# Optimization experiments

Measured on AMD Instinct MI355X. Metric: run time of the kernel, lower is better.

The kernel has to match this reference:

```python
import jax, jax.numpy as jnp
import numpy as np

B, D, DM, K, KA = 4096, 64, 256, 32, 16


def setup_inputs() -> dict:
    key = jax.random.key(0)
    ks = jax.random.split(key, 20)
    rn = lambda i, shape, s=1.0: jax.random.normal(ks[i], shape, dtype=jnp.float32) * s
    return dict(
        z=rn(0, (B, D)),
        rw=jax.random.uniform(ks[1], (B, K), dtype=jnp.float32),
        action_z=rn(2, (B, D)),
        action_rw=jax.random.uniform(ks[3], (B, KA), dtype=jnp.float32),
        action_code_z=rn(4, (B, D)),
        control=rn(5, (B, D)),
        exact_covector=rn(6, (B, D)),
        chart_emb=rn(7, (K, DM), 0.05),
        chart_anchor=rn(8, (K, D)),
        action_chart_emb=rn(9, (KA, DM), 0.05),
        action_chart_anchor=rn(10, (KA, D)),
        z_embed_W=rn(11, (D, DM), 0.05), z_embed_b=jnp.zeros((DM,), jnp.float32),
        lat_W=rn(12, (D, DM), 0.05), lat_b=jnp.zeros((DM,), jnp.float32),
        code_W=rn(13, (D, DM), 0.05), code_b=jnp.zeros((DM,), jnp.float32),
        Wq=rn(14, (DM, DM), 0.05), Wk=rn(15, (DM, DM), 0.05),
        Wv=rn(16, (DM, DM), 0.05), Wo=rn(17, (DM, DM), 0.05),
        form_W=rn(18, (DM, D), 0.05), form_b=jnp.zeros((D,), jnp.float32),
    )


def _spectral_linear(x, W, b):
    # SpectralLinear: weight normalized by its largest singular value.
    sigma = jnp.linalg.svd(W, compute_uv=False)[0]
    return x @ (W / jnp.maximum(sigma, jnp.float32(1e-8))) + b


def _forward(z, rw, action_z, action_rw, action_code_z, control, exact_covector,
             chart_emb, chart_anchor, action_chart_emb, action_chart_anchor,
             z_embed_W, z_embed_b, lat_W, lat_b, code_W, code_b,
             Wq, Wk, Wv, Wo, form_W, form_b):
    b = z.shape[0]
    # ChartTokenizer: routing-weighted chart embeddings + anchor latents.
    chart_x = rw[:, :, None] * chart_emb[None]                      # [B,K,DM]
    chart_z = jnp.broadcast_to(chart_anchor[None], (b, K, D))       # [B,K,D]
    a_chart_x = action_rw[:, :, None] * action_chart_emb[None]      # [B,KA,DM]
    a_chart_z = jnp.broadcast_to(action_chart_anchor[None], (b, KA, D))
    # LatentTokenizers: single token per latent.
    lat_x = (action_z @ lat_W + lat_b)[:, None, :]                  # [B,1,DM]
    code_x = (action_code_z @ code_W + code_b)[:, None, :]          # [B,1,DM]
    ctx_x = jnp.concatenate([lat_x, code_x, a_chart_x, chart_x], axis=1)   # [B,S,DM]
    ctx_z = jnp.concatenate([action_z[:, None], action_code_z[:, None], a_chart_z, chart_z], axis=1)  # [B,S,D]
    # CovariantAttention (1 head): feature scores biased by latent-space distance.
    x_q = z @ z_embed_W + z_embed_b                                 # [B,DM]
    q = x_q @ Wq                                                    # [B,DM]
    k = jnp.einsum('bsd,de->bse', ctx_x, Wk)                        # [B,S,DM]
    v = jnp.einsum('bsd,de->bse', ctx_x, Wv)
    dist2 = jnp.sum((z[:, None, :] - ctx_z) ** 2, axis=-1)          # [B,S]
    scores = jnp.einsum('bd,bsd->bs', q, k) / jnp.sqrt(jnp.float32(DM)) - dist2
    attn = jax.nn.softmax(scores, axis=-1)
    feat = jnp.einsum('bs,bsd->bd', attn, v) @ Wo                   # [B,DM]
    # Residual reward one-form, projected off the (detached) exact direction.
    form_raw = _spectral_linear(feat, form_W, form_b)               # [B,D]
    e = jax.lax.stop_gradient(exact_covector)
    e_norm2 = jnp.sum(e * e, axis=-1, keepdims=True)
    coeff = jnp.where(e_norm2 > 1e-8,
                      jnp.sum(form_raw * e, axis=-1, keepdims=True) / jnp.maximum(e_norm2, 1e-8),
                      jnp.zeros_like(e_norm2))
    form_cov = form_raw - coeff * e
    # Non-conservative scalar reward contribution.
    return jnp.sum(form_cov * control, axis=-1, keepdims=True)      # [B,1]


def reference(z, rw, action_z, action_rw, action_code_z, control, exact_covector,
              chart_emb, chart_anchor, action_chart_emb, action_chart_anchor,
              z_embed_W, z_embed_b, lat_W, lat_b, code_W, code_b,
              Wq, Wk, Wv, Wo, form_W, form_b):
    return _forward(z, rw, action_z, action_rw, action_code_z, control, exact_covector,
                    chart_emb, chart_anchor, action_chart_emb, action_chart_anchor,
                    z_embed_W, z_embed_b, lat_W, lat_b, code_W, code_b,
                    Wq, Wk, Wv, Wo, form_W, form_b)
```

## Files before the change

### kernel.cpp

```cpp
#include <hip/hip_runtime.h>

#define B_N 4096
#define TB 8
#define SQUARINGS 8

#define OFF_W5T  0
#define OFF_B5   81920
#define OFF_KALL 83200
#define OFF_VALL 95488
#define OFF_ANC  107776
#define OFF_M    110848
#define OFF_G    127232
#define OFF_RS   131328
#define OFF_A    131392
#define OFF_Bc   135488

#define S_ZS    0
#define S_AZS   544
#define S_ACZS  1088
#define S_RWS   1632
#define S_ARWS  1920
#define S_QFP   2080
#define S_SW    4160
#define S_RED   4576
#define S_MST   4704
#define SMEM_K2 13200

__global__ __launch_bounds__(256)
void k1_fold(const float* __restrict__ chart_emb, const float* __restrict__ a_chart_emb,
             const float* __restrict__ zW, const float* __restrict__ zb,
             const float* __restrict__ latW, const float* __restrict__ latb,
             const float* __restrict__ codeW, const float* __restrict__ codeb,
             const float* __restrict__ Wq, const float* __restrict__ Wk,
             const float* __restrict__ Wv, const float* __restrict__ Wo,
             const float* __restrict__ fW, const float* __restrict__ ach_anchor,
             const float* __restrict__ ch_anchor, float* __restrict__ ws) {
  __shared__ float red[256];
  const int t = threadIdx.x;
  const int b = blockIdx.x;

  if (b == 2004) {
    for (int e = t; e < 3072; e += 256) {
      int s = e >> 6, d = e & 63;
      ws[OFF_ANC + e] = (s < 16) ? ach_anchor[s * 64 + d] : ch_anchor[(s - 16) * 64 + d];
    }
    return;
  }

  const float* Arow; const float* Bm;
  int astride = 1, bstride = 256, jbase = 0, dstBase, dstStride = 1;
  if (b < 1300) {
    int u = b / 260, r = b - u * 260;
    int i = r >> 2, jc = r & 3; jbase = jc * 64;
    const float* Amat = (u == 0) ? zW : (u <= 2 ? latW : codeW);
    const float* bias = (u == 0) ? zb : (u <= 2 ? latb : codeb);
    Bm = (u == 0) ? Wq : ((u == 1 || u == 3) ? Wk : Wv);
    if (i < 64) {
      Arow = Amat + i * 256;
      dstBase = OFF_W5T + u * 16384 + jbase * 64 + i;
      dstStride = 64;
    } else {
      Arow = bias;
      dstBase = OFF_B5 + u * 256 + jbase;
    }
  } else if (b < 1684) {
    int rr = b - 1300; int row = rr >> 2, jc = rr & 3; jbase = jc * 64;
    int s = (row < 48) ? row : row - 48;
    Bm = (row < 48) ? Wk : Wv;
    Arow = (s < 16) ? (a_chart_emb + s * 256) : (chart_emb + (s - 16) * 256);
    dstBase = OFF_KALL + row * 256 + jbase;
  } else if (b < 1940) {
    int i = b - 1684;
    Arow = Wo + i * 256; Bm = fW; bstride = 64;
    dstBase = OFF_M + i * 64;
  } else {
    int i = b - 1940;
    Arow = fW + i; astride = 64; Bm = fW; bstride = 64;
    dstBase = OFF_G + i * 64;
  }

  const int j = t & 63, ks = t >> 6;
  const float* ap = Arow + (ks * 64) * astride;
  const float* bp = Bm + (ks * 64) * bstride + jbase + j;
  float a0 = 0.f, a1 = 0.f, a2 = 0.f, a3 = 0.f;
  #pragma unroll 4
  for (int k = 0; k < 64; k += 4) {
    a0 += ap[(k + 0) * astride] * bp[(k + 0) * bstride];
    a1 += ap[(k + 1) * astride] * bp[(k + 1) * bstride];
    a2 += ap[(k + 2) * astride] * bp[(k + 2) * bstride];
    a3 += ap[(k + 3) * astride] * bp[(k + 3) * bstride];
  }
  red[t] = (a0 + a1) + (a2 + a3);
  __syncthreads();
  if (t < 64) {
    float v = red[t] + red[64 + t] + red[128 + t] + red[192 + t];
    ws[dstBase + t * dstStride] = v;
  }
}

__device__ __forceinline__ void mv(const float* __restrict__ ws, int u,
                                   const float* xs, int t, float* r) {
  const float* w = ws + OFF_W5T + u * 16384 + t * 64;
  float bq = ws[OFF_B5 + u * 256 + t];
  #pragma unroll
  for (int bi = 0; bi < TB; ++bi) r[bi] = bq;
  #pragma unroll 4
  for (int k4 = 0; k4 < 16; ++k4) {
    float4 w4 = *(const float4*)(w + k4 * 4);
    #pragma unroll
    for (int bi = 0; bi < TB; ++bi) {
      float4 x4 = *(const float4*)&xs[bi * 68 + k4 * 4];
      r[bi] += x4.x * w4.x + x4.y * w4.y + x4.z * w4.z + x4.w * w4.w;
    }
  }
}

__global__ __launch_bounds__(256, 4)
void k2_main(const float* __restrict__ z, const float* __restrict__ rw,
             const float* __restrict__ az, const float* __restrict__ arw,
             const float* __restrict__ acz, const float* __restrict__ ctrl,
             const float* __restrict__ ecov, const float* __restrict__ fb,
             float* __restrict__ ws) {
  __shared__ __align__(16) float sm[SMEM_K2];
  const int t = threadIdx.x;
  const int wv = t >> 6, ln = t & 63;

  if (blockIdx.x == 512) {
    float* GO = sm;
    float* HA = sm + 4352;
    float* HB = sm + 8704;
    for (int e = t; e < 4096; e += 256) {
      int i = e >> 6, j = e & 63;
      GO[i * 68 + j] = ws[OFF_G + e];
    }
    __syncthreads();
    {
      float tv = (t < 64) ? GO[t * 68 + t] : 0.f;
      #pragma unroll
      for (int m = 32; m >= 1; m >>= 1) tv += __shfl_xor(tv, m, 64);
      if (t == 0) sm[13056] = (tv > 0.f) ? 1.f / tv : 0.f;
    }
    __syncthreads();
    {
      float inv0 = sm[13056];
      for (int e = t; e < 4096; e += 256) {
        int i = e >> 6, j = e & 63;
        HA[i * 68 + j] = GO[i * 68 + j] * inv0;
      }
    }
    __syncthreads();
    for (int it = 0; it < SQUARINGS; ++it) {
      float* src = (it & 1) ? HB : HA;
      float* dst = (it & 1) ? HA : HB;
      float acc16[16];
      #pragma unroll
      for (int r = 0; r < 16; ++r) acc16[r] = 0.f;
      for (int half = 0; half < 2; ++half) {
        float cb[32];
        #pragma unroll
        for (int k = 0; k < 32; ++k) cb[k] = src[(half * 32 + k) * 68 + ln];
        #pragma unroll
        for (int r = 0; r < 16; ++r) {
          int i = r * 4 + wv;
          float a = 0.f;
          #pragma unroll
          for (int k4 = 0; k4 < 8; ++k4) {
            float4 a4 = *(const float4*)&src[i * 68 + half * 32 + k4 * 4];
            a += a4.x * cb[k4 * 4] + a4.y * cb[k4 * 4 + 1] + a4.z * cb[k4 * 4 + 2] + a4.w * cb[k4 * 4 + 3];
          }
          acc16[r] += a;
        }
      }
      #pragma unroll
      for (int r = 0; r < 16; ++r) dst[(r * 4 + wv) * 68 + ln] = acc16[r];
      __syncthreads();
      {
        float tv = (t < 64) ? dst[t * 68 + t] : 0.f;
        #pragma unroll
        for (int m = 32; m >= 1; m >>= 1) tv += __shfl_xor(tv, m, 64);
        if (t == 0) sm[13056] = (tv > 0.f) ? 1.f / tv : 0.f;
      }
      __syncthreads();
      {
        float sc = sm[13056];
        #pragma unroll
        for (int r = 0; r < 16; ++r) dst[(r * 4 + wv) * 68 + ln] *= sc;
      }
      __syncthreads();
    }
    float* H = (SQUARINGS & 1) ? HB : HA;
    if (t < 64) {
      float cn = 0.f;
      for (int i = 0; i < 64; ++i) { float h = H[i * 68 + t]; cn += h * h; }
      float bv = cn; int bj = t;
      #pragma unroll
      for (int m = 32; m >= 1; m >>= 1) {
        float ov = __shfl_xor(bv, m, 64);
        int   oj = __shfl_xor(bj, m, 64);
        if (ov > bv || (ov == bv && oj < bj)) { bv = ov; bj = oj; }
      }
      if (t == 0) sm[13057] = (float)bj;
    }
    __syncthreads();
    {
      int jmax = (int)sm[13057];
      if (t < 64) sm[13060 + t] = H[t * 68 + jmax];
    }
    __syncthreads();
    if (t < 64) {
      float vi = sm[13060 + t];
      float y = 0.f;
      #pragma unroll 4
      for (int k = 0; k < 64; ++k) y += GO[t * 68 + k] * sm[13060 + k];
      float num = vi * y, den = vi * vi;
      #pragma unroll
      for (int m = 32; m >= 1; m >>= 1) {
        num += __shfl_xor(num, m, 64);
        den += __shfl_xor(den, m, 64);
      }
      if (t == 0) {
        float lam = (den > 1e-37f) ? num / den : 0.f;
        lam = fmaxf(lam, 0.f);
        float sg = sqrtf(lam);
        ws[OFF_RS] = 1.f / fmaxf(sg, 1e-8f);
      }
    }
    return;
  }

  const int b0 = blockIdx.x * TB;
  for (int e = t; e < TB * 64; e += 256) {
    int bi = e >> 6, d = e & 63; int bb = b0 + bi;
    sm[S_ZS   + bi * 68 + d] = z[bb * 64 + d];
    sm[S_AZS  + bi * 68 + d] = az[bb * 64 + d];
    sm[S_ACZS + bi * 68 + d] = acz[bb * 64 + d];
  }
  { int bi = t >> 5, d = t & 31; sm[S_RWS + bi * 36 + d] = rw[(b0 + bi) * 32 + d]; }
  if (t < 128) { int bi = t >> 4, d = t & 15; sm[S_ARWS + bi * 20 + d] = arw[(b0 + bi) * 16 + d]; }
  __syncthreads();

  float qr[TB];
  mv(ws, 0, sm + S_ZS, t, qr);
  #pragma unroll
  for (int bi = 0; bi < TB; ++bi) sm[S_QFP + bi * 260 + t] = qr[bi];
  {
    float kr[TB];
    mv(ws, 1, sm + S_AZS, t, kr);
    #pragma unroll
    for (int bi = 0; bi < TB; ++bi) {
      float p = qr[bi] * kr[bi];
      #pragma unroll
      for (int m = 32; m >= 1; m >>= 1) p += __shfl_xor(p, m, 64);
      if (ln == 0) sm[S_RED + bi * 16 + wv] = p;
    }
  }
  {
    float kr[TB];
    mv(ws, 3, sm + S_ACZS, t, kr);
    #pragma unroll
    for (int bi = 0; bi < TB; ++bi) {
      float p = qr[bi] * kr[bi];
      #pragma unroll
      for (int m = 32; m >= 1; m >>= 1) p += __shfl_xor(p, m, 64);
      if (ln == 0) sm[S_RED + bi * 16 + 4 + wv] = p;
    }
  }
  if (wv == 0) {
    #pragma unroll
    for (int bi = 0; bi < TB; ++bi) {
      float a = sm[S_ZS + bi * 68 + ln] - sm[S_AZS + bi * 68 + ln];
      float c = sm[S_ZS + bi * 68 + ln] - sm[S_ACZS + bi * 68 + ln];
      float dL = a * a, dC = c * c;
      #pragma unroll
      for (int m = 32; m >= 1; m >>= 1) { dL += __shfl_xor(dL, m, 64); dC += __shfl_xor(dC, m, 64); }
      if (ln == 0) { sm[S_RED + bi * 16 + 8] = dL; sm[S_RED + bi * 16 + 9] = dC; }
    }
  }
  float vlr[TB], vcr[TB];
  mv(ws, 2, sm + S_AZS, t, vlr);
  mv(ws, 4, sm + S_ACZS, t, vcr);
  __syncthreads();

  if (t < TB) {
    float pL = sm[S_RED + t * 16 + 0] + sm[S_RED + t * 16 + 1] + sm[S_RED + t * 16 + 2] + sm[S_RED + t * 16 + 3];
    float pC = sm[S_RED + t * 16 + 4] + sm[S_RED + t * 16 + 5] + sm[S_RED + t * 16 + 6] + sm[S_RED + t * 16 + 7];
    sm[S_SW + t * 52 + 48] = pL * 0.0625f - sm[S_RED + t * 16 + 8];
    sm[S_SW + t * 52 + 49] = pC * 0.0625f - sm[S_RED + t * 16 + 9];
  }

  for (int jb = t; jb < 48 * TB; jb += 256) {
    int s = jb >> 3, bi = jb & 7;
    const float* krow = ws + OFF_KALL + s * 256;
    float dot = 0.f;
    #pragma unroll 4
    for (int k4 = 0; k4 < 64; ++k4) {
      float4 q4 = *(const float4*)&sm[S_QFP + bi * 260 + k4 * 4];
      float4 kk = *(const float4*)(krow + k4 * 4);
      dot += q4.x * kk.x + q4.y * kk.y + q4.z * kk.z + q4.w * kk.w;
    }
    const float* anc = ws + OFF_ANC + s * 64;
    float d2 = 0.f;
    #pragma unroll 4
    for (int k4 = 0; k4 < 16; ++k4) {
      float4 z4 = *(const float4*)&sm[S_ZS + bi * 68 + k4 * 4];
      float4 a4 = *(const float4*)(anc + k4 * 4);
      float d0 = z4.x - a4.x, d1 = z4.y - a4.y, dd = z4.z - a4.z, d3 = z4.w - a4.w;
      d2 += d0 * d0 + d1 * d1 + dd * dd + d3 * d3;
    }
    float rwv = (s < 16) ? sm[S_ARWS + bi * 20 + s] : sm[S_RWS + bi * 36 + (s - 16)];
    sm[S_SW + bi * 52 + s] = rwv * dot * 0.0625f - d2;
  }
  __syncthreads();

  if (t < TB) {
    float* swr = &sm[S_SW + t * 52];
    float mx = -1e30f;
    for (int s = 0; s < 50; ++s) mx = fmaxf(mx, swr[s]);
    float sum = 0.f;
    for (int s = 0; s < 50; ++s) { float ev = __expf(swr[s] - mx); swr[s] = ev; sum += ev; }
    float inv = 1.f / sum;
    for (int j = 0; j < 16; ++j) swr[j]      *= inv * sm[S_ARWS + t * 20 + j];
    for (int k = 0; k < 32; ++k) swr[16 + k] *= inv * sm[S_RWS + t * 36 + k];
    swr[48] *= inv;
    swr[49] *= inv;
  }
  __syncthreads();

  {
    float acc[TB];
    #pragma unroll
    for (int bi = 0; bi < TB; ++bi)
      acc[bi] = sm[S_SW + bi * 52 + 48] * vlr[bi] + sm[S_SW + bi * 52 + 49] * vcr[bi];
    for (int sc = 0; sc < 12; ++sc) {
      float v0 = ws[OFF_VALL + (sc * 4 + 0) * 256 + t];
      float v1 = ws[OFF_VALL + (sc * 4 + 1) * 256 + t];
      float v2 = ws[OFF_VALL + (sc * 4 + 2) * 256 + t];
      float v3 = ws[OFF_VALL + (sc * 4 + 3) * 256 + t];
      #pragma unroll
      for (int bi = 0; bi < TB; ++bi) {
        float4 w4 = *(const float4*)&sm[S_SW + bi * 52 + sc * 4];
        acc[bi] += w4.x * v0 + w4.y * v1 + w4.z * v2 + w4.w * v3;
      }
    }
    __syncthreads();
    #pragma unroll
    for (int bi = 0; bi < TB; ++bi) sm[S_QFP + bi * 260 + t] = acc[bi];
  }
  __syncthreads();

  float g0 = 0.f, g1 = 0.f;
  const int d = ln;
  for (int tc = 0; tc < 4; ++tc) {
    __syncthreads();
    for (int e = t * 4; e < 4096; e += 1024) {
      int kr = e >> 6, dd = e & 63;
      *(float4*)&sm[S_MST + kr * 68 + dd] = *(const float4*)(ws + OFF_M + (tc * 64 + kr) * 64 + dd);
    }
    __syncthreads();
    #pragma unroll 4
    for (int k4 = 0; k4 < 16; ++k4) {
      float m0 = sm[S_MST + (k4 * 4 + 0) * 68 + d];
      float m1 = sm[S_MST + (k4 * 4 + 1) * 68 + d];
      float m2 = sm[S_MST + (k4 * 4 + 2) * 68 + d];
      float m3 = sm[S_MST + (k4 * 4 + 3) * 68 + d];
      float4 f0 = *(const float4*)&sm[S_QFP + wv * 260 + tc * 64 + k4 * 4];
      float4 f1 = *(const float4*)&sm[S_QFP + (wv + 4) * 260 + tc * 64 + k4 * 4];
      g0 += f0.x * m0 + f0.y * m1 + f0.z * m2 + f0.w * m3;
      g1 += f1.x * m0 + f1.y * m1 + f1.z * m2 + f1.w * m3;
    }
  }

  {
    float fbv = fb[d];
    #pragma unroll
    for (int s = 0; s < 2; ++s) {
      float g = (s == 0) ? g0 : g1;
      int bi = wv + s * 4;
      int bb = b0 + bi;
      float c = ctrl[bb * 64 + d];
      float e = ecov[bb * 64 + d];
      float gc = g * c, ge = g * e, ec = e * c, ee = e * e, fc = fbv * c, fe = fbv * e;
      #pragma unroll
      for (int m = 32; m >= 1; m >>= 1) {
        gc += __shfl_xor(gc, m, 64);
        ge += __shfl_xor(ge, m, 64);
        ec += __shfl_xor(ec, m, 64);
        ee += __shfl_xor(ee, m, 64);
        fc += __shfl_xor(fc, m, 64);
        fe += __shfl_xor(fe, m, 64);
      }
      if (ln == 0) {
        float A, Bv;
        if (ee > 1e-8f) { float r = ec / ee; A = gc - ge * r; Bv = fc - fe * r; }
        else { A = gc; Bv = fc; }
        ws[OFF_A  + bb] = A;
        ws[OFF_Bc + bb] = Bv;
      }
    }
  }
}

__global__ __launch_bounds__(256)
void k3_out(const float* __restrict__ ws, float* __restrict__ out) {
  int b = blockIdx.x * 256 + threadIdx.x;
  float rs = ws[OFF_RS];
  out[b] = ws[OFF_A + b] * rs + ws[OFF_Bc + b];
}

extern "C" void kernel_launch(void* const* d_in, const int* in_sizes, int n_in,
                              void* d_out, int out_size, void* d_ws, size_t ws_size,
                              hipStream_t stream) {
  const float* z     = (const float*)d_in[0];
  const float* rw    = (const float*)d_in[1];
  const float* az    = (const float*)d_in[2];
  const float* arw   = (const float*)d_in[3];
  const float* acz   = (const float*)d_in[4];
  const float* ctrl  = (const float*)d_in[5];
  const float* ecov  = (const float*)d_in[6];
  const float* chemb = (const float*)d_in[7];
  const float* chanc = (const float*)d_in[8];
  const float* aemb  = (const float*)d_in[9];
  const float* aanc  = (const float*)d_in[10];
  const float* zW    = (const float*)d_in[11];
  const float* zb    = (const float*)d_in[12];
  const float* latW  = (const float*)d_in[13];
  const float* latb  = (const float*)d_in[14];
  const float* codeW = (const float*)d_in[15];
  const float* codeb = (const float*)d_in[16];
  const float* Wq    = (const float*)d_in[17];
  const float* Wk    = (const float*)d_in[18];
  const float* Wv    = (const float*)d_in[19];
  const float* Wo    = (const float*)d_in[20];
  const float* fW    = (const float*)d_in[21];
  const float* fb    = (const float*)d_in[22];
  float* ws  = (float*)d_ws;
  float* out = (float*)d_out;

  k1_fold<<<2005, 256, 0, stream>>>(chemb, aemb, zW, zb, latW, latb, codeW, codeb,
                                    Wq, Wk, Wv, Wo, fW, aanc, chanc, ws);
  k2_main<<<513, 256, 0, stream>>>(z, rw, az, arw, acz, ctrl, ecov, fb, ws);
  k3_out<<<16, 256, 0, stream>>>(ws, out);
}
```

Baseline: 191.3 us.

## Halve per-block batch tile, read inputs from global, transpose M tile in LDS

Reduces rows per block in the main kernel from 8 to 4 and doubles the grid, so more blocks are available to fill CUs. Input rows and routing weights are read straight from global (broadcast/cached) instead of being staged in shared memory, and the anchor copy block in the fold kernel is removed by reading anchors directly. The M tile is stored transposed with padding and the spectral-norm block reads G from global, which shrinks LDS use and raises occupancy. The trade-off is that each block loads the folded weights for fewer rows, so weight reuse is lower and there are more global reads.

```diff
diff --git a/kernel.cpp b/kernel.cpp
--- a/kernel.cpp
+++ b/kernel.cpp
@@ -1,30 +1,24 @@
 #include <hip/hip_runtime.h>
 
 #define B_N 4096
-#define TB 8
+#define TB 4
 #define SQUARINGS 8
 
 #define OFF_W5T  0
 #define OFF_B5   81920
 #define OFF_KALL 83200
 #define OFF_VALL 95488
-#define OFF_ANC  107776
 #define OFF_M    110848
 #define OFF_G    127232
 #define OFF_RS   131328
 #define OFF_A    131392
 #define OFF_Bc   135488
 
-#define S_ZS    0
-#define S_AZS   544
-#define S_ACZS  1088
-#define S_RWS   1632
-#define S_ARWS  1920
-#define S_QFP   2080
-#define S_SW    4160
-#define S_RED   4576
-#define S_MST   4704
-#define SMEM_K2 13200
+#define S_MT    0
+#define S_QFP   4160
+#define S_SW    5200
+#define S_RED   5408
+#define SMEM_K2 8772
 
 __global__ __launch_bounds__(256)
 void k1_fold(const float* __restrict__ chart_emb, const float* __restrict__ a_chart_emb,
@@ -33,19 +27,10 @@
              const float* __restrict__ codeW, const float* __restrict__ codeb,
              const float* __restrict__ Wq, const float* __restrict__ Wk,
              const float* __restrict__ Wv, const float* __restrict__ Wo,
-             const float* __restrict__ fW, const float* __restrict__ ach_anchor,
-             const float* __restrict__ ch_anchor, float* __restrict__ ws) {
+             const float* __restrict__ fW, float* __restrict__ ws) {
   __shared__ float red[256];
   const int t = threadIdx.x;
   const int b = blockIdx.x;
-
-  if (b == 2004) {
-    for (int e = t; e < 3072; e += 256) {
-      int s = e >> 6, d = e & 63;
-      ws[OFF_ANC + e] = (s < 16) ? ach_anchor[s * 64 + d] : ch_anchor[(s - 16) * 64 + d];
-    }
-    return;
-  }
 
   const float* Arow; const float* Bm;
   int astride = 1, bstride = 256, jbase = 0, dstBase, dstStride = 1;
@@ -99,7 +84,7 @@
 }
 
 __device__ __forceinline__ void mv(const float* __restrict__ ws, int u,
-                                   const float* xs, int t, float* r) {
+                                   const float* __restrict__ xg, int t, float* r) {
   const float* w = ws + OFF_W5T + u * 16384 + t * 64;
   float bq = ws[OFF_B5 + u * 256 + t];
   #pragma unroll
@@ -109,7 +94,7 @@
     float4 w4 = *(const float4*)(w + k4 * 4);
     #pragma unroll
     for (int bi = 0; bi < TB; ++bi) {
-      float4 x4 = *(const float4*)&xs[bi * 68 + k4 * 4];
+      float4 x4 = *(const float4*)(xg + bi * 64 + k4 * 4);
       r[bi] += x4.x * w4.x + x4.y * w4.y + x4.z * w4.z + x4.w * w4.w;
     }
   }
@@ -119,33 +104,28 @@
 void k2_main(const float* __restrict__ z, const float* __restrict__ rw,
              const float* __restrict__ az, const float* __restrict__ arw,
              const float* __restrict__ acz, const float* __restrict__ ctrl,
-             const float* __restrict__ ecov, const float* __restrict__ fb,
+             const float* __restrict__ ecov, const float* __restrict__ chanc,
+             const float* __restrict__ aanc, const float* __restrict__ fb,
              float* __restrict__ ws) {
   __shared__ __align__(16) float sm[SMEM_K2];
   const int t = threadIdx.x;
   const int wv = t >> 6, ln = t & 63;
 
-  if (blockIdx.x == 512) {
-    float* GO = sm;
-    float* HA = sm + 4352;
-    float* HB = sm + 8704;
-    for (int e = t; e < 4096; e += 256) {
-      int i = e >> 6, j = e & 63;
-      GO[i * 68 + j] = ws[OFF_G + e];
-    }
-    __syncthreads();
+  if (blockIdx.x == 1024) {
+    float* HA = sm;
+    float* HB = sm + 4352;
     {
-      float tv = (t < 64) ? GO[t * 68 + t] : 0.f;
+      float tv = (t < 64) ? ws[OFF_G + t * 65] : 0.f;
       #pragma unroll
       for (int m = 32; m >= 1; m >>= 1) tv += __shfl_xor(tv, m, 64);
-      if (t == 0) sm[13056] = (tv > 0.f) ? 1.f / tv : 0.f;
+      if (t == 0) sm[8704] = (tv > 0.f) ? 1.f / tv : 0.f;
     }
     __syncthreads();
     {
-      float inv0 = sm[13056];
+      float inv0 = sm[8704];
       for (int e = t; e < 4096; e += 256) {
         int i = e >> 6, j = e & 63;
-        HA[i * 68 + j] = GO[i * 68 + j] * inv0;
+        HA[i * 68 + j] = ws[OFF_G + e] * inv0;
       }
     }
     __syncthreads();
@@ -178,11 +158,11 @@
         float tv = (t < 64) ? dst[t * 68 + t] : 0.f;
         #pragma unroll
         for (int m = 32; m >= 1; m >>= 1) tv += __shfl_xor(tv, m, 64);
-        if (t == 0) sm[13056] = (tv > 0.f) ? 1.f / tv : 0.f;
+        if (t == 0) sm[8704] = (tv > 0.f) ? 1.f / tv : 0.f;
       }
       __syncthreads();
       {
-        float sc = sm[13056];
+        float sc = sm[8704];
         #pragma unroll
         for (int r = 0; r < 16; ++r) dst[(r * 4 + wv) * 68 + ln] *= sc;
       }
@@ -199,19 +179,19 @@
         int   oj = __shfl_xor(bj, m, 64);
         if (ov > bv || (ov == bv && oj < bj)) { bv = ov; bj = oj; }
       }
-      if (t == 0) sm[13057] = (float)bj;
+      if (t == 0) sm[8705] = (float)bj;
     }
     __syncthreads();
     {
-      int jmax = (int)sm[13057];
-      if (t < 64) sm[13060 + t] = H[t * 68 + jmax];
+      int jmax = (int)sm[8705];
+      if (t < 64) sm[8708 + t] = H[t * 68 + jmax];
     }
     __syncthreads();
     if (t < 64) {
-      float vi = sm[13060 + t];
+      float vi = sm[8708 + t];
       float y = 0.f;
       #pragma unroll 4
-      for (int k = 0; k < 64; ++k) y += GO[t * 68 + k] * sm[13060 + k];
+      for (int k = 0; k < 64; ++k) y += ws[OFF_G + t * 64 + k] * sm[8708 + k];
       float num = vi * y, den = vi * vi;
       #pragma unroll
       for (int m = 32; m >= 1; m >>= 1) {
@@ -229,23 +209,17 @@
   }
 
   const int b0 = blockIdx.x * TB;
-  for (int e = t; e < TB * 64; e += 256) {
-    int bi = e >> 6, d = e & 63; int bb = b0 + bi;
-    sm[S_ZS   + bi * 68 + d] = z[bb * 64 + d];
-    sm[S_AZS  + bi * 68 + d] = az[bb * 64 + d];
-    sm[S_ACZS + bi * 68 + d] = acz[bb * 64 + d];
-  }
-  { int bi = t >> 5, d = t & 31; sm[S_RWS + bi * 36 + d] = rw[(b0 + bi) * 32 + d]; }
-  if (t < 128) { int bi = t >> 4, d = t & 15; sm[S_ARWS + bi * 20 + d] = arw[(b0 + bi) * 16 + d]; }
-  __syncthreads();
+  const float* zg   = z   + b0 * 64;
+  const float* azg  = az  + b0 * 64;
+  const float* aczg = acz + b0 * 64;
 
   float qr[TB];
-  mv(ws, 0, sm + S_ZS, t, qr);
+  mv(ws, 0, zg, t, qr);
   #pragma unroll
   for (int bi = 0; bi < TB; ++bi) sm[S_QFP + bi * 260 + t] = qr[bi];
   {
     float kr[TB];
-    mv(ws, 1, sm + S_AZS, t, kr);
+    mv(ws, 1, azg, t, kr);
     #pragma unroll
     for (int bi = 0; bi < TB; ++bi) {
       float p = qr[bi] * kr[bi];
@@ -256,7 +230,7 @@
   }
   {
     float kr[TB];
-    mv(ws, 3, sm + S_ACZS, t, kr);
+    mv(ws, 3, aczg, t, kr);
     #pragma unroll
     for (int bi = 0; bi < TB; ++bi) {
       float p = qr[bi] * kr[bi];
@@ -268,8 +242,9 @@
   if (wv == 0) {
     #pragma unroll
     for (int bi = 0; bi < TB; ++bi) {
-      float a = sm[S_ZS + bi * 68 + ln] - sm[S_AZS + bi * 68 + ln];
-      float c = sm[S_ZS + bi * 68 + ln] - sm[S_ACZS + bi * 68 + ln];
+      float zv = zg[bi * 64 + ln];
+      float a = zv - azg[bi * 64 + ln];
+      float c = zv - aczg[bi * 64 + ln];
       float dL = a * a, dC = c * c;
       #pragma unroll
       for (int m = 32; m >= 1; m >>= 1) { dL += __shfl_xor(dL, m, 64); dC += __shfl_xor(dC, m, 64); }
@@ -277,8 +252,8 @@
     }
   }
   float vlr[TB], vcr[TB];
-  mv(ws, 2, sm + S_AZS, t, vlr);
-  mv(ws, 4, sm + S_ACZS, t, vcr);
+  mv(ws, 2, azg, t, vlr);
+  mv(ws, 4, aczg, t, vcr);
   __syncthreads();
 
   if (t < TB) {
@@ -288,8 +263,8 @@
     sm[S_SW + t * 52 + 49] = pC * 0.0625f - sm[S_RED + t * 16 + 9];
   }
 
-  for (int jb = t; jb < 48 * TB; jb += 256) {
-    int s = jb >> 3, bi = jb & 7;
+  if (t < 48 * TB) {
+    int s = t >> 2, bi = t & 3;
     const float* krow = ws + OFF_KALL + s * 256;
     float dot = 0.f;
     #pragma unroll 4
@@ -298,16 +273,17 @@
       float4 kk = *(const float4*)(krow + k4 * 4);
       dot += q4.x * kk.x + q4.y * kk.y + q4.z * kk.z + q4.w * kk.w;
     }
-    const float* anc = ws + OFF_ANC + s * 64;
+    const float* anc = (s < 16) ? (aanc + s * 64) : (chanc + (s - 16) * 64);
+    const float* zrow = zg + bi * 64;
     float d2 = 0.f;
     #pragma unroll 4
     for (int k4 = 0; k4 < 16; ++k4) {
-      float4 z4 = *(const float4*)&sm[S_ZS + bi * 68 + k4 * 4];
+      float4 z4 = *(const float4*)(zrow + k4 * 4);
       float4 a4 = *(const float4*)(anc + k4 * 4);
       float d0 = z4.x - a4.x, d1 = z4.y - a4.y, dd = z4.z - a4.z, d3 = z4.w - a4.w;
       d2 += d0 * d0 + d1 * d1 + dd * dd + d3 * d3;
     }
-    float rwv = (s < 16) ? sm[S_ARWS + bi * 20 + s] : sm[S_RWS + bi * 36 + (s - 16)];
+    float rwv = (s < 16) ? arw[(b0 + bi) * 16 + s] : rw[(b0 + bi) * 32 + (s - 16)];
     sm[S_SW + bi * 52 + s] = rwv * dot * 0.0625f - d2;
   }
   __syncthreads();
@@ -319,8 +295,8 @@
     float sum = 0.f;
     for (int s = 0; s < 50; ++s) { float ev = __expf(swr[s] - mx); swr[s] = ev; sum += ev; }
     float inv = 1.f / sum;
-    for (int j = 0; j < 16; ++j) swr[j]      *= inv * sm[S_ARWS + t * 20 + j];
-    for (int k = 0; k < 32; ++k) swr[16 + k] *= inv * sm[S_RWS + t * 36 + k];
+    for (int j = 0; j < 16; ++j) swr[j]      *= inv * arw[(b0 + t) * 16 + j];
+    for (int k = 0; k < 32; ++k) swr[16 + k] *= inv * rw[(b0 + t) * 32 + k];
     swr[48] *= inv;
     swr[49] *= inv;
   }
@@ -331,6 +307,7 @@
     #pragma unroll
     for (int bi = 0; bi < TB; ++bi)
       acc[bi] = sm[S_SW + bi * 52 + 48] * vlr[bi] + sm[S_SW + bi * 52 + 49] * vcr[bi];
+    #pragma unroll 2
     for (int sc = 0; sc < 12; ++sc) {
       float v0 = ws[OFF_VALL + (sc * 4 + 0) * 256 + t];
       float v1 = ws[OFF_VALL + (sc * 4 + 1) * 256 + t];
@@ -346,56 +323,55 @@
     #pragma unroll
     for (int bi = 0; bi < TB; ++bi) sm[S_QFP + bi * 260 + t] = acc[bi];
   }
-  __syncthreads();
-
-  float g0 = 0.f, g1 = 0.f;
-  const int d = ln;
+
+  float g = 0.f;
   for (int tc = 0; tc < 4; ++tc) {
     __syncthreads();
-    for (int e = t * 4; e < 4096; e += 1024) {
-      int kr = e >> 6, dd = e & 63;
-      *(float4*)&sm[S_MST + kr * 68 + dd] = *(const float4*)(ws + OFF_M + (tc * 64 + kr) * 64 + dd);
+    {
+      int dd = (t & 15) * 4, kr0 = t >> 4;
+      #pragma unroll
+      for (int p = 0; p < 4; ++p) {
+        int kr = kr0 + p * 16;
+        float4 m4 = *(const float4*)(ws + OFF_M + (tc * 64 + kr) * 64 + dd);
+        sm[S_MT + (dd + 0) * 65 + kr] = m4.x;
+        sm[S_MT + (dd + 1) * 65 + kr] = m4.y;
+        sm[S_MT + (dd + 2) * 65 + kr] = m4.z;
+        sm[S_MT + (dd + 3) * 65 + kr] = m4.w;
+      }
     }
     __syncthreads();
     #pragma unroll 4
     for (int k4 = 0; k4 < 16; ++k4) {
-      float m0 = sm[S_MST + (k4 * 4 + 0) * 68 + d];
-      float m1 = sm[S_MST + (k4 * 4 + 1) * 68 + d];
-      float m2 = sm[S_MST + (k4 * 4 + 2) * 68 + d];
-      float m3 = sm[S_MST + (k4 * 4 + 3) * 68 + d];
-      float4 f0 = *(const float4*)&sm[S_QFP + wv * 260 + tc * 64 + k4 * 4];
-      float4 f1 = *(const float4*)&sm[S_QFP + (wv + 4) * 260 + tc * 64 + k4 * 4];
-      g0 += f0.x * m0 + f0.y * m1 + f0.z * m2 + f0.w * m3;
-      g1 += f1.x * m0 + f1.y * m1 + f1.z * m2 + f1.w * m3;
+      float4 f4 = *(const float4*)&sm[S_QFP + wv * 260 + tc * 64 + k4 * 4];
+      float m0 = sm[S_MT + ln * 65 + k4 * 4 + 0];
+      float m1 = sm[S_MT + ln * 65 + k4 * 4 + 1];
+      float m2 = sm[S_MT + ln * 65 + k4 * 4 + 2];
+      float m3 = sm[S_MT + ln * 65 + k4 * 4 + 3];
+      g += f4.x * m0 + f4.y * m1 + f4.z * m2 + f4.w * m3;
     }
   }
 
   {
-    float fbv = fb[d];
-    #pragma unroll
-    for (int s = 0; s < 2; ++s) {
-      float g = (s == 0) ? g0 : g1;
-      int bi = wv + s * 4;
-      int bb = b0 + bi;
-      float c = ctrl[bb * 64 + d];
-      float e = ecov[bb * 64 + d];
-      float gc = g * c, ge = g * e, ec = e * c, ee = e * e, fc = fbv * c, fe = fbv * e;
-      #pragma unroll
-      for (int m = 32; m >= 1; m >>= 1) {
-        gc += __shfl_xor(gc, m, 64);
-        ge += __shfl_xor(ge, m, 64);
-        ec += __shfl_xor(ec, m, 64);
-        ee += __shfl_xor(ee, m, 64);
-        fc += __shfl_xor(fc, m, 64);
-        fe += __shfl_xor(fe, m, 64);
-      }
-      if (ln == 0) {
-        float A, Bv;
-        if (ee > 1e-8f) { float r = ec / ee; A = gc - ge * r; Bv = fc - fe * r; }
-        else { A = gc; Bv = fc; }
-        ws[OFF_A  + bb] = A;
-        ws[OFF_Bc + bb] = Bv;
-      }
+    int bb = b0 + wv;
+    float fbv = fb[ln];
+    float c = ctrl[bb * 64 + ln];
+    float e = ecov[bb * 64 + ln];
+    float gc = g * c, ge = g * e, ec = e * c, ee = e * e, fc = fbv * c, fe = fbv * e;
+    #pragma unroll
+    for (int m = 32; m >= 1; m >>= 1) {
+      gc += __shfl_xor(gc, m, 64);
+      ge += __shfl_xor(ge, m, 64);
+      ec += __shfl_xor(ec, m, 64);
+      ee += __shfl_xor(ee, m, 64);
+      fc += __shfl_xor(fc, m, 64);
+      fe += __shfl_xor(fe, m, 64);
+    }
+    if (ln == 0) {
+      float A, Bv;
+      if (ee > 1e-8f) { float r = ec / ee; A = gc - ge * r; Bv = fc - fe * r; }
+      else { A = gc; Bv = fc; }
+      ws[OFF_A  + bb] = A;
+      ws[OFF_Bc + bb] = Bv;
     }
   }
 }
@@ -436,8 +412,9 @@
   float* ws  = (float*)d_ws;
   float* out = (float*)d_out;
 
-  k1_fold<<<2005, 256, 0, stream>>>(chemb, aemb, zW, zb, latW, latb, codeW, codeb,
-                                    Wq, Wk, Wv, Wo, fW, aanc, chanc, ws);
-  k2_main<<<513, 256, 0, stream>>>(z, rw, az, arw, acz, ctrl, ecov, fb, ws);
+  k1_fold<<<2004, 256, 0, stream>>>(chemb, aemb, zW, zb, latW, latb, codeW, codeb,
+                                    Wq, Wk, Wv, Wo, fW, ws);
+  k2_main<<<1025, 256, 0, stream>>>(z, rw, az, arw, acz, ctrl, ecov,
+                                    chanc, aanc, fb, ws);
   k3_out<<<16, 256, 0, stream>>>(ws, out);
 }
```

Measured after the change: 234.2 us. 22.4% more time.
